# Optimization experiments

Hardware: AMD Instinct MI355X
Metric: run time of the kernel (lower is better)

## Reference

```python
import jax, jax.numpy as jnp
import numpy as np

NELEMS = 1_000_000
FEAT = 128
NSEG = 1024


def setup_inputs() -> dict:
    key = jax.random.key(0)
    k1, k2 = jax.random.split(key)
    memory = jax.random.normal(k1, (NELEMS, FEAT), dtype=jnp.float32)
    m_batch = jnp.sort(jax.random.randint(k2, (NELEMS,), 0, NSEG, dtype=jnp.int64))
    return {"memory": memory, "m_batch": m_batch, "num_segments": NSEG}


def reference(memory, m_batch, num_segments):
    # torch.sparse.sum over dim=1 of a [nbatches, nelems, F] COO tensor built from
    # (batch, arange) indices == per-batch segment sum of memory rows.
    return jax.ops.segment_sum(memory, m_batch, num_segments=num_segments)
```

## Files before the change

kernel.cpp:

```cpp
#include <hip/hip_runtime.h>


#define FEAT 128
#define F4 (FEAT / 4)
#define ROWLANES 16
#define THREADS (F4 * ROWLANES)

typedef float f32x4 __attribute__((ext_vector_type(4)));

__global__ void boundaries_kernel(const int* __restrict__ seg,
                                  int* __restrict__ starts,
                                  int nelems, int nseg) {
    int i = blockIdx.x * blockDim.x + threadIdx.x;
    if (i >= nelems) return;
    int cur = seg[i];
    int prev = (i == 0) ? -1 : seg[i - 1];
    for (int s = prev + 1; s <= cur; ++s) starts[s] = i;
    if (i == nelems - 1) {
        for (int s = cur + 1; s <= nseg; ++s) starts[s] = nelems;
    }
}

__global__ __launch_bounds__(THREADS, 8) void segsum_kernel(
        const f32x4* __restrict__ mem,
        const int* __restrict__ starts,
        f32x4* __restrict__ out) {
    const int b    = blockIdx.x;
    const int lane = threadIdx.x & (F4 - 1);
    const int rl   = threadIdx.x >> 5;

    const int start = starts[b];
    const int end   = starts[b + 1];

    f32x4 a0 = (f32x4)0.f, a1 = (f32x4)0.f, a2 = (f32x4)0.f, a3 = (f32x4)0.f;

    int r = start + rl;
    for (; r + 3 * ROWLANES < end; r += 4 * ROWLANES) {
        f32x4 v0 = __builtin_nontemporal_load(&mem[(size_t)r * F4 + lane]);
        f32x4 v1 = __builtin_nontemporal_load(&mem[(size_t)(r + ROWLANES) * F4 + lane]);
        f32x4 v2 = __builtin_nontemporal_load(&mem[(size_t)(r + 2 * ROWLANES) * F4 + lane]);
        f32x4 v3 = __builtin_nontemporal_load(&mem[(size_t)(r + 3 * ROWLANES) * F4 + lane]);
        a0 += v0; a1 += v1; a2 += v2; a3 += v3;
    }
    for (; r < end; r += ROWLANES) {
        a0 += __builtin_nontemporal_load(&mem[(size_t)r * F4 + lane]);
    }
    a0 += a1; a2 += a3; a0 += a2;

    __shared__ f32x4 red[ROWLANES][F4];
    red[rl][lane] = a0;
    __syncthreads();
    if (rl < 4) {
        f32x4 s = red[rl][lane] + red[rl + 4][lane] +
                  red[rl + 8][lane] + red[rl + 12][lane];
        red[rl][lane] = s;
    }
    __syncthreads();
    if (rl == 0) {
        f32x4 s = red[0][lane] + red[1][lane] + red[2][lane] + red[3][lane];
        out[(size_t)b * F4 + lane] = s;
    }
}

extern "C" void kernel_launch(void* const* d_in, const int* in_sizes, int n_in,
                              void* d_out, int out_size, void* d_ws, size_t ws_size,
                              hipStream_t stream) {
    const f32x4* mem = (const f32x4*)d_in[0];
    const int* seg = (const int*)d_in[1];
    f32x4* out = (f32x4*)d_out;
    int* starts = (int*)d_ws;

    const int nelems = in_sizes[1];
    const int nseg = out_size / FEAT;

    int bblocks = (nelems + 255) / 256;
    boundaries_kernel<<<bblocks, 256, 0, stream>>>(seg, starts, nelems, nseg);

    segsum_kernel<<<nseg, THREADS, 0, stream>>>(mem, starts, out);
}
```

Before: 84.65 us.

## Fuse segment boundary search into segment-sum kernel via wavefront ballot search

Drops the separate boundaries kernel and its workspace array. Each block instead finds its own start and end row in the sorted segment ids. It runs a 32-way search using ballot and popcount, with the two half-wavefronts searching for segment b and segment b+1. This removes one kernel launch and a full pass over the index array. In exchange, each block pays a few dependent global loads before it starts streaming rows.

```diff
diff --git a/kernel.cpp b/kernel.cpp
--- a/kernel.cpp
+++ b/kernel.cpp
@@ -8,29 +8,46 @@
 
 typedef float f32x4 __attribute__((ext_vector_type(4)));
 
-__global__ void boundaries_kernel(const int* __restrict__ seg,
-                                  int* __restrict__ starts,
-                                  int nelems, int nseg) {
-    int i = blockIdx.x * blockDim.x + threadIdx.x;
-    if (i >= nelems) return;
-    int cur = seg[i];
-    int prev = (i == 0) ? -1 : seg[i - 1];
-    for (int s = prev + 1; s <= cur; ++s) starts[s] = i;
-    if (i == nelems - 1) {
-        for (int s = cur + 1; s <= nseg; ++s) starts[s] = nelems;
-    }
-}
-
-__global__ __launch_bounds__(THREADS, 8) void segsum_kernel(
+__global__ __launch_bounds__(THREADS, 8) void segsum_fused(
         const f32x4* __restrict__ mem,
-        const int* __restrict__ starts,
-        f32x4* __restrict__ out) {
+        const int* __restrict__ seg,
+        f32x4* __restrict__ out,
+        int nelems) {
     const int b    = blockIdx.x;
     const int lane = threadIdx.x & (F4 - 1);
     const int rl   = threadIdx.x >> 5;
 
-    const int start = starts[b];
-    const int end   = starts[b + 1];
+    __shared__ int sb[2];
+
+    if (threadIdx.x < 64) {
+        const int half = threadIdx.x >> 5;
+        const int j    = threadIdx.x & 31;
+        const int t    = b + half;
+
+        int lo = 0, len = nelems;
+        #pragma unroll
+        for (int round = 0; round < 4; ++round) {
+            int pos = lo + (int)(((long long)j * len) >> 5);
+            int v = seg[pos];
+            unsigned long long m = __ballot(v < t);
+            unsigned mh = half ? (unsigned)(m >> 32) : (unsigned)(m & 0xffffffffull);
+            int c = __popc(mh);
+            int pcm1 = lo + (int)(((long long)(c - 1) * len) >> 5);
+            int pc   = (c < 32) ? (lo + (int)(((long long)c * len) >> 5)) : (lo + len);
+            int newlo = (c > 0) ? pcm1 : lo;
+            int newhi = (c > 0) ? pc : lo;
+            lo = newlo;
+            len = newhi - newlo;
+        }
+        int v = (j < len) ? seg[lo + j] : 0x7fffffff;
+        unsigned long long m = __ballot(v < t);
+        unsigned mh = half ? (unsigned)(m >> 32) : (unsigned)(m & 0xffffffffull);
+        if (j == 0) sb[half] = lo + __popc(mh);
+    }
+    __syncthreads();
+
+    const int start = sb[0];
+    const int end   = sb[1];
 
     f32x4 a0 = (f32x4)0.f, a1 = (f32x4)0.f, a2 = (f32x4)0.f, a3 = (f32x4)0.f;
 
@@ -51,9 +68,8 @@
     red[rl][lane] = a0;
     __syncthreads();
     if (rl < 4) {
-        f32x4 s = red[rl][lane] + red[rl + 4][lane] +
-                  red[rl + 8][lane] + red[rl + 12][lane];
-        red[rl][lane] = s;
+        red[rl][lane] = red[rl][lane] + red[rl + 4][lane] +
+                        red[rl + 8][lane] + red[rl + 12][lane];
     }
     __syncthreads();
     if (rl == 0) {
@@ -68,13 +84,9 @@
     const f32x4* mem = (const f32x4*)d_in[0];
     const int* seg = (const int*)d_in[1];
     f32x4* out = (f32x4*)d_out;
-    int* starts = (int*)d_ws;
 
     const int nelems = in_sizes[1];
     const int nseg = out_size / FEAT;
 
-    int bblocks = (nelems + 255) / 256;
-    boundaries_kernel<<<bblocks, 256, 0, stream>>>(seg, starts, nelems, nseg);
-
-    segsum_kernel<<<nseg, THREADS, 0, stream>>>(mem, starts, out);
+    segsum_fused<<<nseg, THREADS, 0, stream>>>(mem, seg, out, nelems);
 }
```

New measurement: 81.57 us, median of 2. 1.04x faster.
